# Performance work log

Hardware: AMD Instinct MI355X
Metric: run time of the kernel (lower is better)

Reference implementation:

```python
import jax, jax.numpy as jnp
import numpy as np

B, C, E, H = 8, 2048, 1024, 128


def setup_inputs() -> dict:
    key = jax.random.key(0)
    k1, k2, k3, k4 = jax.random.split(key, 4)
    x = jax.random.normal(k1, (B, C, E), dtype=jnp.float32)
    # store projection weights as (E, H) so projection is x @ W
    Wq = jax.random.normal(k2, (E, H), dtype=jnp.float32) * (E ** -0.5)
    Wk = jax.random.normal(k3, (E, H), dtype=jnp.float32) * (E ** -0.5)
    Wv = jax.random.normal(k4, (E, H), dtype=jnp.float32) * (E ** -0.5)
    return {"x": x, "Wq": Wq, "Wk": Wk, "Wv": Wv}


def reference(x, Wq, Wk, Wv):
    # x: (B, C, E) -> out: (B, C, H)
    _, c, e = x.shape
    q = x @ Wq  # (B, C, H)
    k = x @ Wk  # (B, C, H)
    v = x @ Wv  # (B, C, H)
    # NOTE: original scales by embed_size**0.5, not head_size**0.5
    scale = jnp.asarray(e, x.dtype) ** 0.5
    w = jnp.einsum('bqh,bkh->bqk', q, k) / scale  # (B, C, C)
    causal = jnp.tril(jnp.ones((c, c), dtype=bool))
    w = jnp.where(causal, w, -jnp.inf)
    w = jax.nn.softmax(w, axis=-1)
    # dropout_rate = 0.0 -> identity (eval mode)
    out = w @ v  # (B, C, H)
    return out
```

## Files before the change

kernel.cpp:

```cpp
#include <hip/hip_runtime.h>
#include <hip/hip_bf16.h>
#include <stdint.h>

#define B_ 8
#define C_ 2048
#define E_ 1024
#define H_ 128
#define M_ (B_*C_)
#define SLOTS_B 144

typedef __attribute__((ext_vector_type(8))) short bf16x8;
typedef __attribute__((ext_vector_type(4))) float f32x4;

__device__ __forceinline__ unsigned short f2bf(float f) {
    union { float f; unsigned int u; } v; v.f = f;
    unsigned int u = v.u;
    u += 0x7fff + ((u >> 16) & 1);
    return (unsigned short)(u >> 16);
}
__device__ __forceinline__ float bf2f(unsigned short u) {
    union { unsigned int i; float f; } v; v.i = ((unsigned int)u) << 16; return v.f;
}

#define GLOAD_LDS16(g, l) \
    __builtin_amdgcn_global_load_lds((const __attribute__((address_space(1))) void*)(g), \
                                     (__attribute__((address_space(3))) void*)(l), 16, 0, 0)

__global__ __launch_bounds__(256) void wt2_kernel(const float* __restrict__ Wq,
                                                  const float* __restrict__ Wk,
                                                  const float* __restrict__ Wv,
                                                  unsigned short* __restrict__ WT2) {
    int z = blockIdx.y;
    const float* W = (z == 0) ? Wq : (z == 1) ? Wk : Wv;
    unsigned short* o = WT2 + (size_t)z * H_ * E_;
    int gid = blockIdx.x * 256 + threadIdx.x;
    int g = gid >> 7, h = gid & 127;
    unsigned short t[8];
#pragma unroll
    for (int j = 0; j < 8; ++j)
        t[j] = f2bf(W[(size_t)(g * 8 + j) * H_ + h]);
    *(bf16x8*)&o[(size_t)(g * 128 + h) * 8] = *(const bf16x8*)t;
}

#define MF(a, b, c) __builtin_amdgcn_mfma_f32_16x16x32_bf16((a), (b), (c), 0, 0, 0)

#define ALOAD(S, T) { const float* xs_ = xrow + (T) * 64; \
    a##S##_0 = *(const float4*)xs_;  a##S##_1 = *(const float4*)(xs_ + 4); }

#define AWRITE(S, BUF) { \
    unsigned short t_[8] = {f2bf(a##S##_0.x), f2bf(a##S##_0.y), f2bf(a##S##_0.z), f2bf(a##S##_0.w), \
                            f2bf(a##S##_1.x), f2bf(a##S##_1.y), f2bf(a##S##_1.z), f2bf(a##S##_1.w)}; \
    *(bf16x8*)&As[BUF][arow][(ag ^ (arow & 7)) * 8] = *(const bf16x8*)t_; }

#define BLOAD(S, T) { const unsigned short* wp_ = wbase + (size_t)(T) * 8192; \
    b##S##0  = *(const bf16x8*)(wp_);            b##S##1  = *(const bf16x8*)(wp_ + 128); \
    b##S##2  = *(const bf16x8*)(wp_ + 4096);     b##S##3  = *(const bf16x8*)(wp_ + 4224); \
    b##S##4  = *(const bf16x8*)(wp_ + 131072);   b##S##5  = *(const bf16x8*)(wp_ + 131200); \
    b##S##6  = *(const bf16x8*)(wp_ + 135168);   b##S##7  = *(const bf16x8*)(wp_ + 135296); \
    b##S##8  = *(const bf16x8*)(wp_ + 262144);   b##S##9  = *(const bf16x8*)(wp_ + 262272); \
    b##S##10 = *(const bf16x8*)(wp_ + 266240);   b##S##11 = *(const bf16x8*)(wp_ + 266368); }

#define COMPUTE(BUF, S) { \
    bf16x8 af00 = *(const bf16x8*)&As[BUF][ra0][(lq ^ (ra0 & 7)) * 8]; \
    bf16x8 af10 = *(const bf16x8*)&As[BUF][ra1][(lq ^ (ra1 & 7)) * 8]; \
    acc[0][0][0] = MF(af00, b##S##0, acc[0][0][0]);  acc[0][1][0] = MF(af10, b##S##0, acc[0][1][0]); \
    acc[0][0][1] = MF(af00, b##S##1, acc[0][0][1]);  acc[0][1][1] = MF(af10, b##S##1, acc[0][1][1]); \
    acc[1][0][0] = MF(af00, b##S##4, acc[1][0][0]);  acc[1][1][0] = MF(af10, b##S##4, acc[1][1][0]); \
    acc[1][0][1] = MF(af00, b##S##5, acc[1][0][1]);  acc[1][1][1] = MF(af10, b##S##5, acc[1][1][1]); \
    acc[2][0][0] = MF(af00, b##S##8, acc[2][0][0]);  acc[2][1][0] = MF(af10, b##S##8, acc[2][1][0]); \
    acc[2][0][1] = MF(af00, b##S##9, acc[2][0][1]);  acc[2][1][1] = MF(af10, b##S##9, acc[2][1][1]); \
    bf16x8 af01 = *(const bf16x8*)&As[BUF][ra0][((4 + lq) ^ (ra0 & 7)) * 8]; \
    bf16x8 af11 = *(const bf16x8*)&As[BUF][ra1][((4 + lq) ^ (ra1 & 7)) * 8]; \
    acc[0][0][0] = MF(af01, b##S##2, acc[0][0][0]);  acc[0][1][0] = MF(af11, b##S##2, acc[0][1][0]); \
    acc[0][0][1] = MF(af01, b##S##3, acc[0][0][1]);  acc[0][1][1] = MF(af11, b##S##3, acc[0][1][1]); \
    acc[1][0][0] = MF(af01, b##S##6, acc[1][0][0]);  acc[1][1][0] = MF(af11, b##S##6, acc[1][1][0]); \
    acc[1][0][1] = MF(af01, b##S##7, acc[1][0][1]);  acc[1][1][1] = MF(af11, b##S##7, acc[1][1][1]); \
    acc[2][0][0] = MF(af01, b##S##10, acc[2][0][0]); acc[2][1][0] = MF(af11, b##S##10, acc[2][1][0]); \
    acc[2][0][1] = MF(af01, b##S##11, acc[2][0][1]); acc[2][1][1] = MF(af11, b##S##11, acc[2][1][1]); }

#define STEP_E(K) { __syncthreads(); \
    if ((K) < 15) { ALOAD(O, (K)+1); BLOAD(O, (K)+1); } \
    COMPUTE((K)&1, E); \
    if ((K) < 15) AWRITE(O, ((K)+1)&1); }

#define STEP_O(K) { __syncthreads(); \
    if ((K) < 15) { ALOAD(E, (K)+1); BLOAD(E, (K)+1); } \
    COMPUTE((K)&1, O); \
    if ((K) < 15) AWRITE(E, ((K)+1)&1); }

__global__ __launch_bounds__(256) void proj_kernel(const float* __restrict__ x,
                                                   const unsigned short* __restrict__ WT2,
                                                   unsigned short* __restrict__ QKV) {
    __shared__ __align__(16) unsigned short As[2][32][64];

    const int tid = threadIdx.x;
    const int wid = tid >> 6, lane = tid & 63;
    const int lrow = lane & 15, lq = lane >> 4;
    const int wcol = wid * 32;
    const int row0 = blockIdx.x * 32;

    const int arow = tid >> 3;
    const int ag = tid & 7;
    const float* xrow = x + (size_t)(row0 + arow) * E_ + ag * 8;
    const int ra0 = lrow, ra1 = 16 + lrow;
    const unsigned short* wbase = WT2 + (size_t)(lq * 128 + wcol + lrow) * 8;

    f32x4 acc[3][2][2];
#pragma unroll
    for (int w = 0; w < 3; ++w)
#pragma unroll
        for (int mi = 0; mi < 2; ++mi)
#pragma unroll
            for (int ni = 0; ni < 2; ++ni) acc[w][mi][ni] = (f32x4){0.f, 0.f, 0.f, 0.f};

    float4 aE_0, aE_1, aO_0, aO_1;
    bf16x8 bE0, bE1, bE2, bE3, bE4, bE5, bE6, bE7, bE8, bE9, bE10, bE11;
    bf16x8 bO0, bO1, bO2, bO3, bO4, bO5, bO6, bO7, bO8, bO9, bO10, bO11;

    ALOAD(E, 0); BLOAD(E, 0);
    AWRITE(E, 0);

    STEP_E(0)  STEP_O(1)  STEP_E(2)  STEP_O(3)
    STEP_E(4)  STEP_O(5)  STEP_E(6)  STEP_O(7)
    STEP_E(8)  STEP_O(9)  STEP_E(10) STEP_O(11)
    STEP_E(12) STEP_O(13) STEP_E(14) STEP_O(15)

#pragma unroll
    for (int w = 0; w < 2; ++w) {
        const float qs = (w == 0) ? 0.03125f : 1.0f;
        unsigned short* outp = QKV + (size_t)w * M_ * H_;
#pragma unroll
        for (int mi = 0; mi < 2; ++mi) {
            int r0 = row0 + mi * 16 + lq * 4;
#pragma unroll
            for (int ni = 0; ni < 2; ++ni) {
                int col = wcol + ni * 16 + lrow;
#pragma unroll
                for (int r = 0; r < 4; ++r)
                    outp[(size_t)(r0 + r) * H_ + col] = f2bf(acc[w][mi][ni][r] * qs);
            }
        }
    }
    {
        unsigned short* vt = QKV + (size_t)2 * M_ * H_;
        int b = row0 / C_;
        int cbase = row0 % C_;
#pragma unroll
        for (int mi = 0; mi < 2; ++mi) {
            int c0 = cbase + mi * 16 + lq * 4;
#pragma unroll
            for (int ni = 0; ni < 2; ++ni) {
                int h = wcol + ni * 16 + lrow;
                __align__(8) unsigned short p[4] = {f2bf(acc[2][mi][ni][0]), f2bf(acc[2][mi][ni][1]),
                                                    f2bf(acc[2][mi][ni][2]), f2bf(acc[2][mi][ni][3])};
                *(uint2*)&vt[((size_t)b * H_ + h) * C_ + c0] = *(const uint2*)p;
            }
        }
    }
}

__global__ __launch_bounds__(256) void attn_kernel(const unsigned short* __restrict__ QKV,
                                                   unsigned short* __restrict__ PO,
                                                   float* __restrict__ ML,
                                                   float* __restrict__ out) {
    __shared__ __align__(16) unsigned short Ks[2][64][128];
    __shared__ __align__(16) unsigned short Vt[2][128][64];
    __shared__ __align__(16) unsigned short Ps[4][16][72];

    const unsigned short* Q  = QKV;
    const unsigned short* K  = QKV + (size_t)M_ * H_;
    const unsigned short* VT = QKV + (size_t)2 * M_ * H_;

    const int tid = threadIdx.x, wid = tid >> 6, lane = tid & 63;
    const int lrow = lane & 15, lq = lane >> 4, lk = lq * 8;
    const int b = blockIdx.x;
    const int rr = blockIdx.y;

    int j = 0;
#pragma unroll
    for (int jj = 1; jj < 32; ++jj) {
        int q = jj >> 2, s = jj & 3;
        if (jj + 2 * q * (q - 1) + s * q <= rr) j = jj;
    }
    const int qj = j >> 2, sj = j & 3;
    const int Cj = j + 2 * qj * (qj - 1) + sj * qj;
    const int c = rr - Cj;
    const int nch = qj + 1;
    const int t0 = c * 4;
    const int t1 = min(t0 + 4, j + 1);

    const int q0w = j * 64 + wid * 16;
    const unsigned short* Kb  = K  + (size_t)b * C_ * H_;
    const unsigned short* VTb = VT + (size_t)b * H_ * C_;
    const int qrow0 = q0w + lq * 4;

    const int krow = tid >> 4, kg = tid & 15;
    const int vrow = tid >> 3, vg = tid & 7;

    bf16x8 qf[4];
#pragma unroll
    for (int kf = 0; kf < 4; ++kf)
        qf[kf] = *(const bf16x8*)&Q[((size_t)b * C_ + q0w + lrow) * H_ + kf * 32 + lk];

    f32x4 o[8];
#pragma unroll
    for (int nf = 0; nf < 8; ++nf) o[nf] = (f32x4){0.f, 0.f, 0.f, 0.f};
    float m[4] = {-INFINITY, -INFINITY, -INFINITY, -INFINITY};
    float l[4] = {0.f, 0.f, 0.f, 0.f};

    auto STAGE = [&](int buf, int t) {
        const int kv0 = t * 64;
#pragma unroll
        for (int s = 0; s < 4; ++s) {
            int r = s * 16 + krow;
            GLOAD_LDS16(&Kb[(size_t)(kv0 + r) * H_ + ((kg ^ (r & 15)) * 8)],
                        (char*)&Ks[buf][0][0] + s * 4096 + tid * 16);
        }
#pragma unroll
        for (int s = 0; s < 4; ++s) {
            int h = s * 32 + vrow;
            GLOAD_LDS16(&VTb[(size_t)h * C_ + kv0 + ((vg ^ (h & 7)) * 8)],
                        (char*)&Vt[buf][0][0] + s * 4096 + tid * 16);
        }
    };

    STAGE(0, t0);

    for (int t = t0; t < t1; ++t) {
        const int cur = (t - t0) & 1;
        __syncthreads();
        if (t + 1 < t1) STAGE(cur ^ 1, t + 1);

        const int kv0 = t * 64;
        f32x4 s[4];
        __builtin_amdgcn_s_setprio(1);
#pragma unroll
        for (int nf = 0; nf < 4; ++nf) {
            s[nf] = (f32x4){0.f, 0.f, 0.f, 0.f};
            const int rk = nf * 16 + lrow;
#pragma unroll
            for (int kf = 0; kf < 4; ++kf) {
                bf16x8 kb = *(const bf16x8*)&Ks[cur][rk][((kf * 4 + lq) ^ (rk & 15)) * 8];
                s[nf] = __builtin_amdgcn_mfma_f32_16x16x32_bf16(qf[kf], kb, s[nf], 0, 0, 0);
            }
        }
        __builtin_amdgcn_s_setprio(0);
        bf16x8 vb[8][2];
#pragma unroll
        for (int nf = 0; nf < 8; ++nf) {
            const int h = nf * 16 + lrow;
#pragma unroll
            for (int kf2 = 0; kf2 < 2; ++kf2)
                vb[nf][kf2] = *(const bf16x8*)&Vt[cur][h][((kf2 * 4 + lq) ^ (h & 7)) * 8];
        }

        if (t == j) {
#pragma unroll
            for (int nf = 0; nf < 4; ++nf) {
                int key = kv0 + nf * 16 + lrow;
#pragma unroll
                for (int r = 0; r < 4; ++r)
                    if (key > qrow0 + r) s[nf][r] = -INFINITY;
            }
        }
        float mt[4] = {-INFINITY, -INFINITY, -INFINITY, -INFINITY};
#pragma unroll
        for (int nf = 0; nf < 4; ++nf)
#pragma unroll
            for (int r = 0; r < 4; ++r) mt[r] = fmaxf(mt[r], s[nf][r]);
#pragma unroll
        for (int r = 0; r < 4; ++r)
#pragma unroll
            for (int off = 1; off < 16; off <<= 1)
                mt[r] = fmaxf(mt[r], __shfl_xor(mt[r], off));

        float corr[4];
#pragma unroll
        for (int r = 0; r < 4; ++r) {
            float mn = fmaxf(m[r], mt[r]);
            corr[r] = __expf(m[r] - mn);
            m[r] = mn;
        }
        float ps[4] = {0.f, 0.f, 0.f, 0.f};
#pragma unroll
        for (int nf = 0; nf < 4; ++nf)
#pragma unroll
            for (int r = 0; r < 4; ++r) {
                float p = __expf(s[nf][r] - m[r]);
                ps[r] += p;
                Ps[wid][lq * 4 + r][nf * 16 + lrow] = f2bf(p);
            }
#pragma unroll
        for (int r = 0; r < 4; ++r) {
#pragma unroll
            for (int off = 1; off < 16; off <<= 1) ps[r] += __shfl_xor(ps[r], off);
            l[r] = l[r] * corr[r] + ps[r];
        }
#pragma unroll
        for (int nf = 0; nf < 8; ++nf)
#pragma unroll
            for (int r = 0; r < 4; ++r) o[nf][r] *= corr[r];

        bf16x8 pa[2];
#pragma unroll
        for (int kf2 = 0; kf2 < 2; ++kf2)
            pa[kf2] = *(const bf16x8*)&Ps[wid][lrow][kf2 * 32 + lk];
        __builtin_amdgcn_s_setprio(1);
#pragma unroll
        for (int nf = 0; nf < 8; ++nf)
#pragma unroll
            for (int kf2 = 0; kf2 < 2; ++kf2)
                o[nf] = __builtin_amdgcn_mfma_f32_16x16x32_bf16(pa[kf2], vb[nf][kf2], o[nf], 0, 0, 0);
        __builtin_amdgcn_s_setprio(0);
    }

    if (nch == 1) {
#pragma unroll
        for (int nf = 0; nf < 8; ++nf) {
            int col = nf * 16 + lrow;
#pragma unroll
            for (int r = 0; r < 4; ++r)
                out[((size_t)b * C_ + qrow0 + r) * H_ + col] = o[nf][r] / l[r];
        }
    } else {
        const int slot = b * SLOTS_B + rr;
        unsigned short* po = PO + (size_t)slot * 64 * 128;
        const int rl0 = wid * 16 + lq * 4;
#pragma unroll
        for (int nf = 0; nf < 8; ++nf) {
            int col = nf * 16 + lrow;
#pragma unroll
            for (int r = 0; r < 4; ++r)
                po[(size_t)(rl0 + r) * 128 + col] = f2bf(o[nf][r]);
        }
        if (lrow == 0) {
            float* ml = ML + (size_t)slot * 128;
#pragma unroll
            for (int r = 0; r < 4; ++r) {
                ml[rl0 + r] = m[r];
                ml[64 + rl0 + r] = l[r];
            }
        }
    }
}

__global__ __launch_bounds__(256) void combine_kernel(const unsigned short* __restrict__ PO,
                                                      const float* __restrict__ ML,
                                                      float* __restrict__ out) {
    const int j = blockIdx.x + 4;
    const int b = blockIdx.y;
    const int q = j >> 2, s = j & 3;
    const int Cj = j + 2 * q * (q - 1) + s * q;
    const int nch = q + 1;
    const int base = b * SLOTS_B + Cj;
    const int row = threadIdx.x >> 2;
    const int colg = (threadIdx.x & 3) * 32;

    float mstar = -INFINITY;
    for (int c = 0; c < nch; ++c)
        mstar = fmaxf(mstar, ML[(size_t)(base + c) * 128 + row]);

    float denom = 0.f;
    float acc[32];
#pragma unroll
    for (int i = 0; i < 32; ++i) acc[i] = 0.f;

    for (int c = 0; c < nch; ++c) {
        float mc = ML[(size_t)(base + c) * 128 + row];
        float lc = ML[(size_t)(base + c) * 128 + 64 + row];
        float w = __expf(mc - mstar);
        denom += w * lc;
        const unsigned short* p = PO + (size_t)(base + c) * 64 * 128 + (size_t)row * 128 + colg;
#pragma unroll
        for (int k = 0; k < 4; ++k) {
            bf16x8 v = *(const bf16x8*)&p[k * 8];
#pragma unroll
            for (int e = 0; e < 8; ++e)
                acc[k * 8 + e] += w * bf2f(((unsigned short*)&v)[e]);
        }
    }
    float inv = 1.f / denom;
    float* op = out + ((size_t)b * C_ + j * 64 + row) * H_ + colg;
#pragma unroll
    for (int k = 0; k < 8; ++k) {
        float4 st = {acc[k * 4] * inv, acc[k * 4 + 1] * inv, acc[k * 4 + 2] * inv, acc[k * 4 + 3] * inv};
        *(float4*)&op[k * 4] = st;
    }
}

extern "C" void kernel_launch(void* const* d_in, const int* in_sizes, int n_in,
                              void* d_out, int out_size, void* d_ws, size_t ws_size,
                              hipStream_t stream) {
    const float* x  = (const float*)d_in[0];
    const float* Wq = (const float*)d_in[1];
    const float* Wk = (const float*)d_in[2];
    const float* Wv = (const float*)d_in[3];
    float* out = (float*)d_out;

    unsigned short* WT2 = (unsigned short*)d_ws;
    unsigned short* QKV = WT2 + (size_t)3 * H_ * E_;
    unsigned short* PO  = QKV + (size_t)3 * M_ * H_;
    float*          ML  = (float*)(PO + (size_t)8 * SLOTS_B * 64 * 128);

    wt2_kernel<<<dim3(E_ / 8 * H_ / 256, 3), 256, 0, stream>>>(Wq, Wk, Wv, WT2);
    proj_kernel<<<dim3(M_ / 32), 256, 0, stream>>>(x, WT2, QKV);
    attn_kernel<<<dim3(B_, SLOTS_B), 256, 0, stream>>>(QKV, PO, ML, out);
    combine_kernel<<<dim3(28, B_), 256, 0, stream>>>(PO, ML, out);
}
```

Measured before the change: 76.27 us.

## Compute transposed S tile to keep softmax probabilities in registers

Result: faster. 70.12 us (median of 2 runs) (-8.1%).

```diff
diff --git a/kernel.cpp b/kernel.cpp
--- a/kernel.cpp
+++ b/kernel.cpp
@@ -20,6 +20,10 @@
 }
 __device__ __forceinline__ float bf2f(unsigned short u) {
     union { unsigned int i; float f; } v; v.i = ((unsigned int)u) << 16; return v.f;
+}
+__device__ __forceinline__ unsigned int pack2bf(float lo, float hi) {
+    union { float f; unsigned int u; } a, b; a.f = lo; b.f = hi;
+    return __builtin_amdgcn_perm(b.u + 0x8000u, a.u + 0x8000u, 0x07060302);
 }
 
 #define GLOAD_LDS16(g, l) \
@@ -165,7 +169,6 @@
                                                    float* __restrict__ out) {
     __shared__ __align__(16) unsigned short Ks[2][64][128];
     __shared__ __align__(16) unsigned short Vt[2][128][64];
-    __shared__ __align__(16) unsigned short Ps[4][16][72];
 
     const unsigned short* Q  = QKV;
     const unsigned short* K  = QKV + (size_t)M_ * H_;
@@ -192,7 +195,7 @@
     const int q0w = j * 64 + wid * 16;
     const unsigned short* Kb  = K  + (size_t)b * C_ * H_;
     const unsigned short* VTb = VT + (size_t)b * H_ * C_;
-    const int qrow0 = q0w + lq * 4;
+    const int qabs = q0w + lrow;
 
     const int krow = tid >> 4, kg = tid & 15;
     const int vrow = tid >> 3, vg = tid & 7;
@@ -205,15 +208,15 @@
     f32x4 o[8];
 #pragma unroll
     for (int nf = 0; nf < 8; ++nf) o[nf] = (f32x4){0.f, 0.f, 0.f, 0.f};
-    float m[4] = {-INFINITY, -INFINITY, -INFINITY, -INFINITY};
-    float l[4] = {0.f, 0.f, 0.f, 0.f};
+    float m = -INFINITY, l = 0.f;
 
     auto STAGE = [&](int buf, int t) {
         const int kv0 = t * 64;
 #pragma unroll
         for (int s = 0; s < 4; ++s) {
             int r = s * 16 + krow;
-            GLOAD_LDS16(&Kb[(size_t)(kv0 + r) * H_ + ((kg ^ (r & 15)) * 8)],
+            int prow = ((r & 0x10) << 1) | ((r & 0x0C) << 1) | ((r & 0x20) >> 3) | (r & 3);
+            GLOAD_LDS16(&Kb[(size_t)(kv0 + prow) * H_ + ((kg ^ (r & 15)) * 8)],
                         (char*)&Ks[buf][0][0] + s * 4096 + tid * 16);
         }
 #pragma unroll
@@ -241,7 +244,7 @@
 #pragma unroll
             for (int kf = 0; kf < 4; ++kf) {
                 bf16x8 kb = *(const bf16x8*)&Ks[cur][rk][((kf * 4 + lq) ^ (rk & 15)) * 8];
-                s[nf] = __builtin_amdgcn_mfma_f32_16x16x32_bf16(qf[kf], kb, s[nf], 0, 0, 0);
+                s[nf] = __builtin_amdgcn_mfma_f32_16x16x32_bf16(kb, qf[kf], s[nf], 0, 0, 0);
             }
         }
         __builtin_amdgcn_s_setprio(0);
@@ -257,54 +260,57 @@
         if (t == j) {
 #pragma unroll
             for (int nf = 0; nf < 4; ++nf) {
-                int key = kv0 + nf * 16 + lrow;
+                int kvb = kv0 + ((nf & 1) << 5) + (lq << 3) + ((nf >> 1) << 2);
 #pragma unroll
                 for (int r = 0; r < 4; ++r)
-                    if (key > qrow0 + r) s[nf][r] = -INFINITY;
-            }
-        }
-        float mt[4] = {-INFINITY, -INFINITY, -INFINITY, -INFINITY};
+                    if (kvb + r > qabs) s[nf][r] = -INFINITY;
+            }
+        }
+        float mt = s[0][0];
 #pragma unroll
         for (int nf = 0; nf < 4; ++nf)
 #pragma unroll
-            for (int r = 0; r < 4; ++r) mt[r] = fmaxf(mt[r], s[nf][r]);
+            for (int r = 0; r < 4; ++r) mt = fmaxf(mt, s[nf][r]);
+        mt = fmaxf(mt, __shfl_xor(mt, 16));
+        mt = fmaxf(mt, __shfl_xor(mt, 32));
+
+        float mn = fmaxf(m, mt);
+        float corr = __expf(m - mn);
+        m = mn;
+
+        float p[4][4];
+        float ps = 0.f;
+#pragma unroll
+        for (int nf = 0; nf < 4; ++nf)
+#pragma unroll
+            for (int r = 0; r < 4; ++r) {
+                float e = __expf(s[nf][r] - mn);
+                p[nf][r] = e;
+                ps += e;
+            }
+        ps += __shfl_xor(ps, 16);
+        ps += __shfl_xor(ps, 32);
+        l = l * corr + ps;
+
+        float corr4[4];
 #pragma unroll
         for (int r = 0; r < 4; ++r)
-#pragma unroll
-            for (int off = 1; off < 16; off <<= 1)
-                mt[r] = fmaxf(mt[r], __shfl_xor(mt[r], off));
-
-        float corr[4];
-#pragma unroll
-        for (int r = 0; r < 4; ++r) {
-            float mn = fmaxf(m[r], mt[r]);
-            corr[r] = __expf(m[r] - mn);
-            m[r] = mn;
-        }
-        float ps[4] = {0.f, 0.f, 0.f, 0.f};
-#pragma unroll
-        for (int nf = 0; nf < 4; ++nf)
-#pragma unroll
-            for (int r = 0; r < 4; ++r) {
-                float p = __expf(s[nf][r] - m[r]);
-                ps[r] += p;
-                Ps[wid][lq * 4 + r][nf * 16 + lrow] = f2bf(p);
-            }
-#pragma unroll
-        for (int r = 0; r < 4; ++r) {
-#pragma unroll
-            for (int off = 1; off < 16; off <<= 1) ps[r] += __shfl_xor(ps[r], off);
-            l[r] = l[r] * corr[r] + ps[r];
-        }
+            corr4[r] = __shfl(corr, (lane & 48) | (lq * 4 + r));
 #pragma unroll
         for (int nf = 0; nf < 8; ++nf)
 #pragma unroll
-            for (int r = 0; r < 4; ++r) o[nf][r] *= corr[r];
+            for (int r = 0; r < 4; ++r) o[nf][r] *= corr4[r];
 
         bf16x8 pa[2];
 #pragma unroll
-        for (int kf2 = 0; kf2 < 2; ++kf2)
-            pa[kf2] = *(const bf16x8*)&Ps[wid][lrow][kf2 * 32 + lk];
+        for (int kf2 = 0; kf2 < 2; ++kf2) {
+            union { unsigned int u[4]; bf16x8 v; } pk;
+            pk.u[0] = pack2bf(p[kf2][0],     p[kf2][1]);
+            pk.u[1] = pack2bf(p[kf2][2],     p[kf2][3]);
+            pk.u[2] = pack2bf(p[kf2 + 2][0], p[kf2 + 2][1]);
+            pk.u[3] = pack2bf(p[kf2 + 2][2], p[kf2 + 2][3]);
+            pa[kf2] = pk.v;
+        }
         __builtin_amdgcn_s_setprio(1);
 #pragma unroll
         for (int nf = 0; nf < 8; ++nf)
@@ -314,13 +320,21 @@
         __builtin_amdgcn_s_setprio(0);
     }
 
+    float l4[4], m4[4];
+#pragma unroll
+    for (int r = 0; r < 4; ++r) {
+        l4[r] = __shfl(l, (lane & 48) | (lq * 4 + r));
+        m4[r] = __shfl(m, (lane & 48) | (lq * 4 + r));
+    }
+    const int qrow0 = q0w + lq * 4;
+
     if (nch == 1) {
 #pragma unroll
         for (int nf = 0; nf < 8; ++nf) {
             int col = nf * 16 + lrow;
 #pragma unroll
             for (int r = 0; r < 4; ++r)
-                out[((size_t)b * C_ + qrow0 + r) * H_ + col] = o[nf][r] / l[r];
+                out[((size_t)b * C_ + qrow0 + r) * H_ + col] = o[nf][r] / l4[r];
         }
     } else {
         const int slot = b * SLOTS_B + rr;
@@ -337,8 +351,8 @@
             float* ml = ML + (size_t)slot * 128;
 #pragma unroll
             for (int r = 0; r < 4; ++r) {
-                ml[rl0 + r] = m[r];
-                ml[64 + rl0 + r] = l[r];
+                ml[rl0 + r] = m4[r];
+                ml[64 + rl0 + r] = l4[r];
             }
         }
     }
```
